# Optimization experiments

Measured on AMD Instinct MI355X. Metric: run time of the kernel, lower is better.

Reference implementation:

```python
import jax, jax.numpy as jnp
import numpy as np
from jax import lax

B, T, D, U, M = 64, 800, 3, 400, 20


def _lstm_peephole(x, Wx, Wh, b, p_i, p_f, p_o):
    """Peephole LSTM over [B,T,Din] -> [B,T,U]. Gate order: i,f,c,o."""
    xW = jnp.einsum('btd,dg->btg', x, Wx) + b  # precompute input projection [B,T,4U]
    h0 = jnp.zeros((x.shape[0], U), x.dtype)
    c0 = jnp.zeros((x.shape[0], U), x.dtype)

    def step(carry, xt):
        h, c = carry
        z = xt + h @ Wh
        zi, zf, zc, zo = jnp.split(z, 4, axis=-1)
        i = jax.nn.sigmoid(zi + p_i * c)
        f = jax.nn.sigmoid(zf + p_f * c)
        c_new = f * c + i * jnp.tanh(zc)
        o = jax.nn.sigmoid(zo + p_o * c_new)
        h_new = o * jnp.tanh(c_new)
        return (h_new, c_new), h_new

    _, hs = lax.scan(step, (h0, c0), jnp.swapaxes(xW, 0, 1))  # [T,B,U]
    return jnp.swapaxes(hs, 0, 1)


def _mdn(h, Wmdn, bmdn):
    y = h @ Wmdn + bmdn  # [B,T,6M+1]
    pi = jax.nn.softmax(y[..., :M], axis=-1)
    mu1 = y[..., M:2 * M]
    mu2 = y[..., 2 * M:3 * M]
    s1 = jnp.exp(y[..., 3 * M:4 * M])
    s2 = jnp.exp(y[..., 4 * M:5 * M])
    rho = jnp.tanh(y[..., 5 * M:6 * M])
    eos = jax.nn.sigmoid(y[..., 6 * M:])
    return jnp.concatenate([pi, mu1, mu2, s1, s2, rho, eos], axis=-1)


def setup_inputs() -> dict:
    key = jax.random.key(0)
    ks = jax.random.split(key, 32)
    s = 0.08
    inp = {'x': jax.random.normal(ks[0], (B, T, D), jnp.float32)}
    k = 1
    for l in range(3):
        din = D if l == 0 else D + U
        inp[f'Wx{l}'] = jax.random.normal(ks[k], (din, 4 * U), jnp.float32) * s; k += 1
        inp[f'Wh{l}'] = jax.random.normal(ks[k], (U, 4 * U), jnp.float32) * s; k += 1
        inp[f'b{l}'] = jnp.zeros((4 * U,), jnp.float32)
        inp[f'peep_i{l}'] = jax.random.normal(ks[k], (U,), jnp.float32) * s; k += 1
        inp[f'peep_f{l}'] = jax.random.normal(ks[k], (U,), jnp.float32) * s; k += 1
        inp[f'peep_o{l}'] = jax.random.normal(ks[k], (U,), jnp.float32) * s; k += 1
    inp['Wmdn'] = jax.random.normal(ks[k], (U, 6 * M + 1), jnp.float32) * s
    inp['bmdn'] = jnp.zeros((6 * M + 1,), jnp.float32)
    return inp


def reference(x, Wx0, Wh0, b0, peep_i0, peep_f0, peep_o0,
              Wx1, Wh1, b1, peep_i1, peep_f1, peep_o1,
              Wx2, Wh2, b2, peep_i2, peep_f2, peep_o2,
              Wmdn, bmdn):
    h = _lstm_peephole(x, Wx0, Wh0, b0, peep_i0, peep_f0, peep_o0)
    # skip connections: layers 1,2 take concat([inputs, prev_hidden])
    h = _lstm_peephole(jnp.concatenate([x, h], axis=-1), Wx1, Wh1, b1, peep_i1, peep_f1, peep_o1)
    h = _lstm_peephole(jnp.concatenate([x, h], axis=-1), Wx2, Wh2, b2, peep_i2, peep_f2, peep_o2)
    return _mdn(h, Wmdn, bmdn)
```

## Files before the change

kernel.cpp:

```cpp
#include <hip/hip_runtime.h>


#define TSTEPS 800
#define NG 4
#define GB 16
#define NSL 5
#define UB 80
#define CB 320
#define KP 416
#define RD 16
#define AS 424
#define ZS 332
#define ZIS 336

typedef __attribute__((ext_vector_type(8))) __bf16 bf16x8;
typedef __attribute__((ext_vector_type(4))) float floatx4;

struct Peeps { const float* pi[3]; const float* pf[3]; const float* po[3]; };

__device__ __forceinline__ unsigned short f2bf(float f) {
    unsigned int u = __float_as_uint(f);
    return (unsigned short)((u + 0x7FFFu + ((u >> 16) & 1u)) >> 16);
}
__device__ __forceinline__ float bf_lo(unsigned u) { return __uint_as_float(u << 16); }
__device__ __forceinline__ float bf_hi(unsigned u) { return __uint_as_float(u & 0xFFFF0000u); }
__device__ __forceinline__ float sigm_(float v) { return 1.f / (1.f + __expf(-v)); }
__device__ __forceinline__ float tanh_(float v) { float e = __expf(2.f * v); return 1.f - 2.f / (e + 1.f); }
__device__ __forceinline__ unsigned ld_a(const unsigned* p) {
    return __hip_atomic_load(p, __ATOMIC_RELAXED, __HIP_MEMORY_SCOPE_AGENT);
}
__device__ __forceinline__ void st_a(unsigned* p, unsigned v) {
    __hip_atomic_store(p, v, __ATOMIC_RELAXED, __HIP_MEMORY_SCOPE_AGENT);
}

__global__ void pack_rec(const float* __restrict__ Wx, const float* __restrict__ Wh,
                         const float* __restrict__ bias, unsigned short* __restrict__ dst,
                         int is_l0) {
    int idx = blockIdx.x * 256 + threadIdx.x;
    if (idx >= 1600 * KP) return;
    int col = idx / KP, k = idx - col * KP;
    int co = (col & 3) * 400 + (col >> 2);
    float v = 0.f;
    if (k < 400) v = Wh[k * 1600 + co];
    else if (is_l0) {
        if (k < 403) v = Wx[(k - 400) * 1600 + co];
        else if (k == 403) v = bias[co];
    }
    dst[idx] = f2bf(v);
}
__global__ void pack_pre(const float* __restrict__ Wx, const float* __restrict__ bias,
                         unsigned short* __restrict__ dst) {
    int idx = blockIdx.x * 256 + threadIdx.x;
    if (idx >= 1600 * KP) return;
    int col = idx / KP, k = idx - col * KP;
    int co = (col & 3) * 400 + (col >> 2);
    float v = 0.f;
    if (k < 400) v = Wx[(3 + k) * 1600 + co];
    else if (k < 403) v = Wx[(k - 400) * 1600 + co];
    else if (k == 403) v = bias[co];
    dst[idx] = f2bf(v);
}
__global__ void pack_x(const float* __restrict__ x, unsigned short* __restrict__ xp) {
    int idx = blockIdx.x * 256 + threadIdx.x;
    if (idx >= TSTEPS * 64) return;
    int t = idx / 64, b = idx - t * 64;
    unsigned short o[4];
    for (int d = 0; d < 3; ++d) o[d] = f2bf(x[(b * TSTEPS + t) * 3 + d]);
    o[3] = 0x3F80u;
    *(uint2*)(xp + (size_t)idx * 4) = *(uint2*)o;
}
__global__ void pack_mdn(const float* __restrict__ Wm, const float* __restrict__ bm,
                         unsigned short* __restrict__ dst) {
    int idx = blockIdx.x * 256 + threadIdx.x;
    if (idx >= 128 * KP) return;
    int col = idx / KP, k = idx - col * KP;
    float v = 0.f;
    if (col < 121) {
        if (k < 400) v = Wm[k * 121 + col];
        else if (k == 400) v = bm[col];
    }
    dst[idx] = f2bf(v);
}

__global__ __launch_bounds__(640)
void fused_scan(const unsigned short* __restrict__ Bp,
                const unsigned short* __restrict__ Bpre,
                const unsigned short* __restrict__ xpack,
                unsigned* __restrict__ ring,
                unsigned* __restrict__ zin,
                unsigned* __restrict__ seqb,
                unsigned short* __restrict__ h2,
                Peeps pp) {
    const int tid = threadIdx.x;
    const int lane = tid & 63;
    const int w = tid >> 6;
    const int bid = blockIdx.x;

    __shared__ unsigned short A[16 * AS];
    __shared__ float Z[16 * ZS];
    __shared__ unsigned short Zin[16 * ZIS];

    for (int i = tid; i < 16 * AS; i += 640) A[i] = 0;

    const int aoff = (lane & 15) * AS + ((lane >> 4) << 3);
    const int zc0 = w * 32 + (lane & 15);
    const int zr = (lane >> 4) << 2;
    const int er = tid / 40;
    const int up = tid - er * 40;

    if (bid < 60) {
        const int l = bid / 20;
        const int g = (bid % 20) / 5;
        const int s = bid % 5;
        bf16x8 breg[2][13];
        #pragma unroll
        for (int n = 0; n < 2; ++n) {
            const unsigned short* bpp = Bp + (size_t)l * 1600 * KP
                + (size_t)(s * CB + w * 32 + n * 16 + (lane & 15)) * KP + ((lane >> 4) << 3);
            #pragma unroll
            for (int kt = 0; kt < 13; ++kt) breg[n][kt] = *(const bf16x8*)(bpp + kt * 32);
        }
        unsigned* hs_own  = seqb + (l * NG + g) * 16;
        const unsigned* ps_up = seqb + 192 + ((l - 1) * NG + g) * 16;
        const unsigned* ps_dn = seqb + 192 + (l * NG + g) * 16;
        unsigned* ringL = ring + (size_t)(l * NG + g) * RD * 3200;
        const unsigned* zinL = zin + (size_t)((l - 1) * NG + g) * RD * 12800;

        const int ug0 = s * UB + 2 * up;
        const float pi0 = pp.pi[l][ug0], pi1 = pp.pi[l][ug0 + 1];
        const float pf0 = pp.pf[l][ug0], pf1 = pp.pf[l][ug0 + 1];
        const float po0 = pp.po[l][ug0], po1 = pp.po[l][ug0 + 1];
        float c0 = 0.f, c1 = 0.f;
        __syncthreads();

        for (int t = 0; t < TSTEPS; ++t) {
            if (w == 0) {
                const unsigned* fp = nullptr; unsigned need = 0;
                if (lane < 5)       { if (t > 0) { fp = hs_own + lane; need = (unsigned)t; } }
                else if (lane < 10) { if (l > 0) { fp = ps_up + (lane - 5); need = (unsigned)(t + 1); } }
                else if (lane < 15) { if (l < 2 && t >= 16 && (t & 7) == 0) { fp = ps_dn + (lane - 10); need = (unsigned)(t - 8); } }
                bool ok = (fp == nullptr) || (ld_a(fp) >= need);
                while (!__all(ok)) { if (!ok) ok = ld_a(fp) >= need; }
            }
            __syncthreads();

            if (t > 0) {
                const unsigned* src = ringL + (size_t)((t - 1) & 15) * 3200;
                for (int i = tid; i < 800; i += 640) {
                    int r = i / 50, c4 = (i - r * 50) * 4;
                    unsigned v0 = ld_a(src + r * 200 + c4);
                    unsigned v1 = ld_a(src + r * 200 + c4 + 1);
                    unsigned v2 = ld_a(src + r * 200 + c4 + 2);
                    unsigned v3 = ld_a(src + r * 200 + c4 + 3);
                    unsigned* dst = (unsigned*)&A[r * AS + c4 * 2];
                    dst[0] = v0; dst[1] = v1; dst[2] = v2; dst[3] = v3;
                }
            }
            if (l == 0 && tid < 16)
                *(uint2*)(&A[tid * AS + 400]) = *(const uint2*)(xpack + ((size_t)t * 64 + g * 16 + tid) * 4);
            if (l > 0) {
                const unsigned* zp = zinL + (size_t)(t & 15) * 12800 + er * 800 + s * 160 + up * 4;
                unsigned z0 = ld_a(zp), z1 = ld_a(zp + 1), z2 = ld_a(zp + 2), z3 = ld_a(zp + 3);
                unsigned* zd = (unsigned*)&Zin[er * ZIS + up * 8];
                zd[0] = z0; zd[1] = z1; zd[2] = z2; zd[3] = z3;
            }
            __syncthreads();

            floatx4 a0 = {0, 0, 0, 0}, a1 = {0, 0, 0, 0};
            #pragma unroll
            for (int kt = 0; kt < 13; ++kt) {
                bf16x8 a = *(const bf16x8*)(&A[aoff + kt * 32]);
                a0 = __builtin_amdgcn_mfma_f32_16x16x32_bf16(a, breg[0][kt], a0, 0, 0, 0);
                a1 = __builtin_amdgcn_mfma_f32_16x16x32_bf16(a, breg[1][kt], a1, 0, 0, 0);
            }
            #pragma unroll
            for (int ri = 0; ri < 4; ++ri) {
                Z[(zr + ri) * ZS + zc0] = a0[ri];
                Z[(zr + ri) * ZS + zc0 + 16] = a1[ri];
            }
            __syncthreads();

            {
                float4 za = *(const float4*)(&Z[er * ZS + 8 * up]);
                float4 zb = *(const float4*)(&Z[er * ZS + 8 * up + 4]);
                if (l > 0) {
                    const unsigned* q = (const unsigned*)&Zin[er * ZIS + 8 * up];
                    unsigned q0 = q[0], q1 = q[1], q2 = q[2], q3 = q[3];
                    za.x += bf_lo(q0); za.y += bf_hi(q0); za.z += bf_lo(q1); za.w += bf_hi(q1);
                    zb.x += bf_lo(q2); zb.y += bf_hi(q2); zb.z += bf_lo(q3); zb.w += bf_hi(q3);
                }
                float iv = sigm_(za.x + pi0 * c0);
                float fv = sigm_(za.y + pf0 * c0);
                float cn = fv * c0 + iv * tanh_(za.z);
                float ov = sigm_(za.w + po0 * cn);
                float h0 = ov * tanh_(cn);
                c0 = cn;
                iv = sigm_(zb.x + pi1 * c1);
                fv = sigm_(zb.y + pf1 * c1);
                cn = fv * c1 + iv * tanh_(zb.z);
                ov = sigm_(zb.w + po1 * cn);
                float h1 = ov * tanh_(cn);
                c1 = cn;
                unsigned packh = (unsigned)f2bf(h0) | ((unsigned)f2bf(h1) << 16);
                st_a(ringL + (size_t)(t & 15) * 3200 + er * 200 + s * 40 + up, packh);
                if (l == 2)
                    *(unsigned*)&h2[(size_t)t * 25600 + (g * GB + er) * 400 + ug0] = packh;
            }
            __syncthreads();
            if (tid == 0) st_a(hs_own + s, (unsigned)(t + 1));
        }
    } else {
        const int p = bid - 60;
        const int lp = 1 + p / 20;
        const int g = (p % 20) / 5;
        const int s = p % 5;
        bf16x8 breg[2][13];
        #pragma unroll
        for (int n = 0; n < 2; ++n) {
            const unsigned short* bpp = Bpre + (size_t)(lp - 1) * 1600 * KP
                + (size_t)(s * CB + w * 32 + n * 16 + (lane & 15)) * KP + ((lane >> 4) << 3);
            #pragma unroll
            for (int kt = 0; kt < 13; ++kt) breg[n][kt] = *(const bf16x8*)(bpp + kt * 32);
        }
        const unsigned* hs_up = seqb + ((lp - 1) * NG + g) * 16;
        const unsigned* hs_cons = seqb + (lp * NG + g) * 16;
        unsigned* pseq = seqb + 192 + ((lp - 1) * NG + g) * 16 + s;
        const unsigned* ringS = ring + (size_t)((lp - 1) * NG + g) * RD * 3200;
        unsigned* zinD = zin + (size_t)((lp - 1) * NG + g) * RD * 12800;
        __syncthreads();

        for (int t = 0; t < TSTEPS; ++t) {
            if (w == 0) {
                const unsigned* fp = nullptr; unsigned need = 0;
                if (lane < 5)       { fp = hs_up + lane; need = (unsigned)(t + 1); }
                else if (lane < 10) { if (t >= 16 && (t & 7) == 0) { fp = hs_cons + (lane - 5); need = (unsigned)(t - 8); } }
                bool ok = (fp == nullptr) || (ld_a(fp) >= need);
                while (!__all(ok)) { if (!ok) ok = ld_a(fp) >= need; }
            }
            __syncthreads();

            {
                const unsigned* src = ringS + (size_t)(t & 15) * 3200;
                for (int i = tid; i < 800; i += 640) {
                    int r = i / 50, c4 = (i - r * 50) * 4;
                    unsigned v0 = ld_a(src + r * 200 + c4);
                    unsigned v1 = ld_a(src + r * 200 + c4 + 1);
                    unsigned v2 = ld_a(src + r * 200 + c4 + 2);
                    unsigned v3 = ld_a(src + r * 200 + c4 + 3);
                    unsigned* dst = (unsigned*)&A[r * AS + c4 * 2];
                    dst[0] = v0; dst[1] = v1; dst[2] = v2; dst[3] = v3;
                }
            }
            if (tid < 16)
                *(uint2*)(&A[tid * AS + 400]) = *(const uint2*)(xpack + ((size_t)t * 64 + g * 16 + tid) * 4);
            __syncthreads();

            floatx4 a0 = {0, 0, 0, 0}, a1 = {0, 0, 0, 0};
            #pragma unroll
            for (int kt = 0; kt < 13; ++kt) {
                bf16x8 a = *(const bf16x8*)(&A[aoff + kt * 32]);
                a0 = __builtin_amdgcn_mfma_f32_16x16x32_bf16(a, breg[0][kt], a0, 0, 0, 0);
                a1 = __builtin_amdgcn_mfma_f32_16x16x32_bf16(a, breg[1][kt], a1, 0, 0, 0);
            }
            #pragma unroll
            for (int ri = 0; ri < 4; ++ri) {
                Z[(zr + ri) * ZS + zc0] = a0[ri];
                Z[(zr + ri) * ZS + zc0 + 16] = a1[ri];
            }
            __syncthreads();

            {
                float4 za = *(const float4*)(&Z[er * ZS + 8 * up]);
                float4 zb = *(const float4*)(&Z[er * ZS + 8 * up + 4]);
                unsigned* zd = zinD + (size_t)(t & 15) * 12800 + er * 800 + s * 160 + up * 4;
                st_a(zd,     (unsigned)f2bf(za.x) | ((unsigned)f2bf(za.y) << 16));
                st_a(zd + 1, (unsigned)f2bf(za.z) | ((unsigned)f2bf(za.w) << 16));
                st_a(zd + 2, (unsigned)f2bf(zb.x) | ((unsigned)f2bf(zb.y) << 16));
                st_a(zd + 3, (unsigned)f2bf(zb.z) | ((unsigned)f2bf(zb.w) << 16));
            }
            __syncthreads();
            if (tid == 0) st_a(pseq, (unsigned)(t + 1));
        }
    }
}

__global__ __launch_bounds__(256)
void mdn_kernel(const unsigned short* __restrict__ h2,
                const unsigned short* __restrict__ Bm,
                float* __restrict__ out) {
    const int blk = blockIdx.x;
    const int b = blk / 25;
    const int t0 = (blk - b * 25) * 32;
    const int tid = threadIdx.x;
    const int lane = tid & 63;
    const int w = tid >> 6;
    const int m = w & 1, nh = w >> 1;

    __shared__ unsigned short A[32 * 424];
    __shared__ float Z[32 * 132];
    __shared__ float rmax[32], rinv[32];

    for (int i = tid; i < 32 * 424; i += 256) A[i] = 0;
    __syncthreads();
    for (int c = tid; c < 32 * 50; c += 256) {
        int r = c / 50, j = c - r * 50;
        *(bf16x8*)(&A[r * 424 + j * 8]) = *(const bf16x8*)(h2 + (size_t)(t0 + r) * 25600 + b * 400 + j * 8);
    }
    if (tid < 32) A[tid * 424 + 400] = 0x3F80u;
    __syncthreads();

    floatx4 acc[4] = {{0,0,0,0},{0,0,0,0},{0,0,0,0},{0,0,0,0}};
    const int aoff = (m * 16 + (lane & 15)) * 424 + ((lane >> 4) << 3);
    #pragma unroll
    for (int kt = 0; kt < 13; ++kt) {
        bf16x8 a = *(const bf16x8*)(&A[aoff + kt * 32]);
        #pragma unroll
        for (int n = 0; n < 4; ++n) {
            const unsigned short* bp = Bm + (size_t)((nh * 4 + n) * 16 + (lane & 15)) * KP
                                          + ((lane >> 4) << 3) + kt * 32;
            acc[n] = __builtin_amdgcn_mfma_f32_16x16x32_bf16(a, *(const bf16x8*)bp, acc[n], 0, 0, 0);
        }
    }
    #pragma unroll
    for (int n = 0; n < 4; ++n) {
        int zc = (nh * 4 + n) * 16 + (lane & 15);
        int zrow = m * 16 + ((lane >> 4) << 2);
        #pragma unroll
        for (int ri = 0; ri < 4; ++ri)
            Z[(zrow + ri) * 132 + zc] = acc[n][ri];
    }
    __syncthreads();
    if (tid < 32) {
        float mx = -1e30f;
        for (int j = 0; j < 20; ++j) mx = fmaxf(mx, Z[tid * 132 + j]);
        float sm = 0.f;
        for (int j = 0; j < 20; ++j) sm += __expf(Z[tid * 132 + j] - mx);
        rmax[tid] = mx;
        rinv[tid] = 1.f / sm;
    }
    __syncthreads();
    for (int idx = tid; idx < 32 * 121; idx += 256) {
        int r = idx / 121, jo = idx - r * 121;
        float v = Z[r * 132 + jo];
        float o;
        if (jo < 20) o = __expf(v - rmax[r]) * rinv[r];
        else if (jo < 60) o = v;
        else if (jo < 100) o = __expf(v);
        else if (jo < 120) o = tanh_(v);
        else o = sigm_(v);
        out[(size_t)(b * TSTEPS + t0 + r) * 121 + jo] = o;
    }
}

extern "C" void kernel_launch(void* const* d_in, const int* in_sizes, int n_in,
                              void* d_out, int out_size, void* d_ws, size_t ws_size,
                              hipStream_t stream) {
    const float* x = (const float*)d_in[0];
    const float* Wx[3] = {(const float*)d_in[1], (const float*)d_in[7], (const float*)d_in[13]};
    const float* Wh[3] = {(const float*)d_in[2], (const float*)d_in[8], (const float*)d_in[14]};
    const float* bb[3] = {(const float*)d_in[3], (const float*)d_in[9], (const float*)d_in[15]};
    Peeps pp;
    for (int l = 0; l < 3; ++l) {
        pp.pi[l] = (const float*)d_in[4 + 6 * l];
        pp.pf[l] = (const float*)d_in[5 + 6 * l];
        pp.po[l] = (const float*)d_in[6 + 6 * l];
    }
    const float* Wm = (const float*)d_in[19];
    const float* bm = (const float*)d_in[20];
    float* out = (float*)d_out;

    char* base = (char*)d_ws;
    size_t off = 0;
    auto alloc = [&](size_t bytes) -> void* {
        void* r = base + off;
        off = (off + bytes + 255) & ~(size_t)255;
        return r;
    };
    unsigned* seqb        = (unsigned*)alloc(320 * sizeof(unsigned));
    unsigned* ring        = (unsigned*)alloc((size_t)3 * NG * RD * 3200 * 4);
    unsigned* zin         = (unsigned*)alloc((size_t)2 * NG * RD * 12800 * 4);
    unsigned short* Bp    = (unsigned short*)alloc((size_t)3 * 1600 * KP * 2);
    unsigned short* Bpre  = (unsigned short*)alloc((size_t)2 * 1600 * KP * 2);
    unsigned short* Bm    = (unsigned short*)alloc((size_t)128 * KP * 2);
    unsigned short* xpk   = (unsigned short*)alloc((size_t)TSTEPS * 64 * 4 * 2);
    unsigned short* h2    = (unsigned short*)alloc((size_t)TSTEPS * 64 * 400 * 2);

    hipMemsetAsync(seqb, 0, 320 * sizeof(unsigned), stream);

    for (int l = 0; l < 3; ++l)
        pack_rec<<<2600, 256, 0, stream>>>(Wx[l], Wh[l], bb[l], Bp + (size_t)l * 1600 * KP, l == 0);
    pack_pre<<<2600, 256, 0, stream>>>(Wx[1], bb[1], Bpre);
    pack_pre<<<2600, 256, 0, stream>>>(Wx[2], bb[2], Bpre + (size_t)1600 * KP);
    pack_x<<<200, 256, 0, stream>>>(x, xpk);
    pack_mdn<<<208, 256, 0, stream>>>(Wm, bm, Bm);

    fused_scan<<<100, 640, 0, stream>>>(Bp, Bpre, xpk, ring, zin, seqb, h2, pp);

    mdn_kernel<<<1600, 256, 0, stream>>>(h2, Bm, out);
}
```

Measured before the change: 3.771 ms.

## Replace per-step sequence flags with tagged hidden-state exchange and batch pre-projection by two

Recurrent blocks now publish each hidden value together with a timestep tag in a small 4-deep exchange buffer. Consumers poll the tagged data directly, which removes the separate flag round-trip and one barrier per step. Each block also writes its own slice of h into LDS locally, and the next x input is prefetched one step ahead. The pre-projection blocks now handle two timesteps per iteration with coarser flags, and the zin load goes straight to registers instead of staging through LDS. The cost is more polling traffic, a larger memset, and more complex ordering that relies on relaxed atomics for correctness.

```diff
diff --git a/kernel.cpp b/kernel.cpp
--- a/kernel.cpp
+++ b/kernel.cpp
@@ -9,9 +9,9 @@
 #define CB 320
 #define KP 416
 #define RD 16
+#define HXD 4
 #define AS 424
 #define ZS 332
-#define ZIS 336
 
 typedef __attribute__((ext_vector_type(8))) __bf16 bf16x8;
 typedef __attribute__((ext_vector_type(4))) float floatx4;
@@ -86,27 +86,27 @@
 void fused_scan(const unsigned short* __restrict__ Bp,
                 const unsigned short* __restrict__ Bpre,
                 const unsigned short* __restrict__ xpack,
-                unsigned* __restrict__ ring,
+                unsigned* __restrict__ hx,
+                unsigned* __restrict__ hring,
                 unsigned* __restrict__ zin,
                 unsigned* __restrict__ seqb,
-                unsigned short* __restrict__ h2,
+                unsigned* __restrict__ h2,
                 Peeps pp) {
     const int tid = threadIdx.x;
     const int lane = tid & 63;
     const int w = tid >> 6;
     const int bid = blockIdx.x;
 
-    __shared__ unsigned short A[16 * AS];
+    __shared__ unsigned short A[32 * AS];
     __shared__ float Z[16 * ZS];
-    __shared__ unsigned short Zin[16 * ZIS];
-
-    for (int i = tid; i < 16 * AS; i += 640) A[i] = 0;
-
+
+    for (int i = tid; i < 32 * AS; i += 640) A[i] = 0;
+
+    const int er = tid / 40;
+    const int up = tid - er * 40;
     const int aoff = (lane & 15) * AS + ((lane >> 4) << 3);
     const int zc0 = w * 32 + (lane & 15);
     const int zr = (lane >> 4) << 2;
-    const int er = tid / 40;
-    const int up = tid - er * 40;
 
     if (bid < 60) {
         const int l = bid / 20;
@@ -120,51 +120,67 @@
             #pragma unroll
             for (int kt = 0; kt < 13; ++kt) breg[n][kt] = *(const bf16x8*)(bpp + kt * 32);
         }
-        unsigned* hs_own  = seqb + (l * NG + g) * 16;
-        const unsigned* ps_up = seqb + 192 + ((l - 1) * NG + g) * 16;
-        const unsigned* ps_dn = seqb + 192 + (l * NG + g) * 16;
-        unsigned* ringL = ring + (size_t)(l * NG + g) * RD * 3200;
+        unsigned* hxL = hx + (size_t)(l * NG + g) * HXD * 6400;
+        unsigned* ringL = hring + (size_t)(l * NG + g) * RD * 3200;
         const unsigned* zinL = zin + (size_t)((l - 1) * NG + g) * RD * 12800;
-
+        unsigned* FHown = seqb + ((l * NG + g) * NSL + s) * 16;
+        const unsigned* FZup = seqb + (60 + ((l - 1) * NG + g) * NSL) * 16;
+        const unsigned* FZdn = seqb + (60 + (l * NG + g) * NSL) * 16;
+
+        const int p0 = ((s + 1) % 5) * 80, p1 = ((s + 2) % 5) * 80;
+        const int p2 = ((s + 3) % 5) * 80, p3 = ((s + 4) % 5) * 80;
         const int ug0 = s * UB + 2 * up;
         const float pi0 = pp.pi[l][ug0], pi1 = pp.pi[l][ug0 + 1];
         const float pf0 = pp.pf[l][ug0], pf1 = pp.pf[l][ug0 + 1];
         const float po0 = pp.po[l][ug0], po1 = pp.po[l][ug0 + 1];
         float c0 = 0.f, c1 = 0.f;
+
         __syncthreads();
+        if (l == 0 && tid < 16)
+            *(uint2*)(&A[tid * AS + 400]) = *(const uint2*)(xpack + ((size_t)0 * 64 + g * 16 + tid) * 4);
+        __syncthreads();
 
         for (int t = 0; t < TSTEPS; ++t) {
-            if (w == 0) {
-                const unsigned* fp = nullptr; unsigned need = 0;
-                if (lane < 5)       { if (t > 0) { fp = hs_own + lane; need = (unsigned)t; } }
-                else if (lane < 10) { if (l > 0) { fp = ps_up + (lane - 5); need = (unsigned)(t + 1); } }
-                else if (lane < 15) { if (l < 2 && t >= 16 && (t & 7) == 0) { fp = ps_dn + (lane - 10); need = (unsigned)(t - 8); } }
-                bool ok = (fp == nullptr) || (ld_a(fp) >= need);
-                while (!__all(ok)) { if (!ok) ok = ld_a(fp) >= need; }
+            {
+                const unsigned want = (unsigned)(t - 1) << 16;
+                const unsigned* hb = hxL + (size_t)((t + 3) & 3) * 6400 + er * 400 + 2 * up;
+                const unsigned* fp = nullptr; unsigned fneed = 0;
+                if (l > 0 && (t & 3) == 0 && tid < NSL) { fp = FZup + tid * 16; fneed = (unsigned)(t + 4); }
+                else if (l < 2 && (t & 7) == 0 && tid >= NSL && tid < 2 * NSL) {
+                    fp = FZdn + (tid - NSL) * 16; fneed = (unsigned)(t > 8 ? t - 8 : 0);
+                }
+                unsigned v0, v1, v2, v3, v4, v5, v6, v7;
+                for (;;) {
+                    bool ok = true;
+                    if (t > 0) {
+                        v0 = ld_a(hb + p0); v1 = ld_a(hb + p0 + 1);
+                        v2 = ld_a(hb + p1); v3 = ld_a(hb + p1 + 1);
+                        v4 = ld_a(hb + p2); v5 = ld_a(hb + p2 + 1);
+                        v6 = ld_a(hb + p3); v7 = ld_a(hb + p3 + 1);
+                        ok = ((v0 & 0xFFFF0000u) == want) & ((v1 & 0xFFFF0000u) == want) &
+                             ((v2 & 0xFFFF0000u) == want) & ((v3 & 0xFFFF0000u) == want) &
+                             ((v4 & 0xFFFF0000u) == want) & ((v5 & 0xFFFF0000u) == want) &
+                             ((v6 & 0xFFFF0000u) == want) & ((v7 & 0xFFFF0000u) == want);
+                    }
+                    if (fp) ok &= (ld_a(fp) >= fneed);
+                    if (__all(ok)) break;
+                }
+                if (t > 0) {
+                    const int ab = er * AS + 2 * up;
+                    *(unsigned*)&A[ab + p0] = (v0 & 0xFFFFu) | (v1 << 16);
+                    *(unsigned*)&A[ab + p1] = (v2 & 0xFFFFu) | (v3 << 16);
+                    *(unsigned*)&A[ab + p2] = (v4 & 0xFFFFu) | (v5 << 16);
+                    *(unsigned*)&A[ab + p3] = (v6 & 0xFFFFu) | (v7 << 16);
+                }
             }
             __syncthreads();
-
-            if (t > 0) {
-                const unsigned* src = ringL + (size_t)((t - 1) & 15) * 3200;
-                for (int i = tid; i < 800; i += 640) {
-                    int r = i / 50, c4 = (i - r * 50) * 4;
-                    unsigned v0 = ld_a(src + r * 200 + c4);
-                    unsigned v1 = ld_a(src + r * 200 + c4 + 1);
-                    unsigned v2 = ld_a(src + r * 200 + c4 + 2);
-                    unsigned v3 = ld_a(src + r * 200 + c4 + 3);
-                    unsigned* dst = (unsigned*)&A[r * AS + c4 * 2];
-                    dst[0] = v0; dst[1] = v1; dst[2] = v2; dst[3] = v3;
-                }
-            }
-            if (l == 0 && tid < 16)
-                *(uint2*)(&A[tid * AS + 400]) = *(const uint2*)(xpack + ((size_t)t * 64 + g * 16 + tid) * 4);
+            if (tid == 0) st_a(FHown, (unsigned)t);
+
+            unsigned q0, q1, q2, q3;
             if (l > 0) {
-                const unsigned* zp = zinL + (size_t)(t & 15) * 12800 + er * 800 + s * 160 + up * 4;
-                unsigned z0 = ld_a(zp), z1 = ld_a(zp + 1), z2 = ld_a(zp + 2), z3 = ld_a(zp + 3);
-                unsigned* zd = (unsigned*)&Zin[er * ZIS + up * 8];
-                zd[0] = z0; zd[1] = z1; zd[2] = z2; zd[3] = z3;
-            }
-            __syncthreads();
+                const unsigned* zp = zinL + (size_t)(t & 15) * 12800 + er * 800 + 4 * (s * 40 + up);
+                q0 = ld_a(zp); q1 = ld_a(zp + 1); q2 = ld_a(zp + 2); q3 = ld_a(zp + 3);
+            }
 
             floatx4 a0 = {0, 0, 0, 0}, a1 = {0, 0, 0, 0};
             #pragma unroll
@@ -180,107 +196,114 @@
             }
             __syncthreads();
 
-            {
-                float4 za = *(const float4*)(&Z[er * ZS + 8 * up]);
-                float4 zb = *(const float4*)(&Z[er * ZS + 8 * up + 4]);
-                if (l > 0) {
-                    const unsigned* q = (const unsigned*)&Zin[er * ZIS + 8 * up];
-                    unsigned q0 = q[0], q1 = q[1], q2 = q[2], q3 = q[3];
-                    za.x += bf_lo(q0); za.y += bf_hi(q0); za.z += bf_lo(q1); za.w += bf_hi(q1);
-                    zb.x += bf_lo(q2); zb.y += bf_hi(q2); zb.z += bf_lo(q3); zb.w += bf_hi(q3);
-                }
-                float iv = sigm_(za.x + pi0 * c0);
-                float fv = sigm_(za.y + pf0 * c0);
-                float cn = fv * c0 + iv * tanh_(za.z);
-                float ov = sigm_(za.w + po0 * cn);
-                float h0 = ov * tanh_(cn);
-                c0 = cn;
-                iv = sigm_(zb.x + pi1 * c1);
-                fv = sigm_(zb.y + pf1 * c1);
-                cn = fv * c1 + iv * tanh_(zb.z);
-                ov = sigm_(zb.w + po1 * cn);
-                float h1 = ov * tanh_(cn);
-                c1 = cn;
-                unsigned packh = (unsigned)f2bf(h0) | ((unsigned)f2bf(h1) << 16);
+            float4 za = *(const float4*)(&Z[er * ZS + 8 * up]);
+            float4 zb4 = *(const float4*)(&Z[er * ZS + 8 * up + 4]);
+            if (l > 0) {
+                za.x += bf_lo(q0); za.y += bf_hi(q0); za.z += bf_lo(q1); za.w += bf_hi(q1);
+                zb4.x += bf_lo(q2); zb4.y += bf_hi(q2); zb4.z += bf_lo(q3); zb4.w += bf_hi(q3);
+            }
+            float iv = sigm_(za.x + pi0 * c0);
+            float fv = sigm_(za.y + pf0 * c0);
+            float cn = fv * c0 + iv * tanh_(za.z);
+            float ov = sigm_(za.w + po0 * cn);
+            float h0 = ov * tanh_(cn);
+            c0 = cn;
+            iv = sigm_(zb4.x + pi1 * c1);
+            fv = sigm_(zb4.y + pf1 * c1);
+            cn = fv * c1 + iv * tanh_(zb4.z);
+            ov = sigm_(zb4.w + po1 * cn);
+            float h1 = ov * tanh_(cn);
+            c1 = cn;
+            unsigned packh = (unsigned)f2bf(h0) | ((unsigned)f2bf(h1) << 16);
+            *(unsigned*)&A[er * AS + ug0] = packh;
+            if (l == 0 && tid < 16 && t + 1 < TSTEPS)
+                *(uint2*)(&A[tid * AS + 400]) = *(const uint2*)(xpack + ((size_t)(t + 1) * 64 + g * 16 + tid) * 4);
+            __syncthreads();
+
+            unsigned* hxs = hxL + (size_t)(t & 3) * 6400 + er * 400 + ug0;
+            st_a(hxs, ((unsigned)t << 16) | (packh & 0xFFFFu));
+            st_a(hxs + 1, ((unsigned)t << 16) | (packh >> 16));
+            if (l < 2)
                 st_a(ringL + (size_t)(t & 15) * 3200 + er * 200 + s * 40 + up, packh);
-                if (l == 2)
-                    *(unsigned*)&h2[(size_t)t * 25600 + (g * GB + er) * 400 + ug0] = packh;
-            }
-            __syncthreads();
-            if (tid == 0) st_a(hs_own + s, (unsigned)(t + 1));
+            else
+                h2[(size_t)t * 12800 + (g * GB + er) * 200 + s * 40 + up] = packh;
         }
+        __syncthreads();
+        if (tid == 0) st_a(FHown, (unsigned)TSTEPS);
     } else {
         const int p = bid - 60;
-        const int lp = 1 + p / 20;
+        const int lz = p / 20;
         const int g = (p % 20) / 5;
-        const int s = p % 5;
+        const int sp = p % 5;
         bf16x8 breg[2][13];
         #pragma unroll
         for (int n = 0; n < 2; ++n) {
-            const unsigned short* bpp = Bpre + (size_t)(lp - 1) * 1600 * KP
-                + (size_t)(s * CB + w * 32 + n * 16 + (lane & 15)) * KP + ((lane >> 4) << 3);
+            const unsigned short* bpp = Bpre + (size_t)lz * 1600 * KP
+                + (size_t)(sp * CB + w * 32 + n * 16 + (lane & 15)) * KP + ((lane >> 4) << 3);
             #pragma unroll
             for (int kt = 0; kt < 13; ++kt) breg[n][kt] = *(const bf16x8*)(bpp + kt * 32);
         }
-        const unsigned* hs_up = seqb + ((lp - 1) * NG + g) * 16;
-        const unsigned* hs_cons = seqb + (lp * NG + g) * 16;
-        unsigned* pseq = seqb + 192 + ((lp - 1) * NG + g) * 16 + s;
-        const unsigned* ringS = ring + (size_t)((lp - 1) * NG + g) * RD * 3200;
-        unsigned* zinD = zin + (size_t)((lp - 1) * NG + g) * RD * 12800;
+        const unsigned* ringS = hring + (size_t)(lz * NG + g) * RD * 3200;
+        unsigned* zinD = zin + (size_t)(lz * NG + g) * RD * 12800;
+        const unsigned* FHup = seqb + ((lz * NG + g) * NSL) * 16;
+        const unsigned* FHdn = seqb + (((lz + 1) * NG + g) * NSL) * 16;
+        unsigned* FZown = seqb + (60 + (lz * NG + g) * NSL + sp) * 16;
         __syncthreads();
 
-        for (int t = 0; t < TSTEPS; ++t) {
-            if (w == 0) {
+        for (int c = 0; c < TSTEPS; c += 2) {
+            {
                 const unsigned* fp = nullptr; unsigned need = 0;
-                if (lane < 5)       { fp = hs_up + lane; need = (unsigned)(t + 1); }
-                else if (lane < 10) { if (t >= 16 && (t & 7) == 0) { fp = hs_cons + (lane - 5); need = (unsigned)(t - 8); } }
+                if (tid < NSL) { fp = FHup + tid * 16; need = (unsigned)(c + 2); }
+                else if (tid < 2 * NSL) { fp = FHdn + (tid - NSL) * 16; need = (unsigned)(c > 14 ? c - 14 : 0); }
                 bool ok = (fp == nullptr) || (ld_a(fp) >= need);
                 while (!__all(ok)) { if (!ok) ok = ld_a(fp) >= need; }
             }
             __syncthreads();
-
-            {
-                const unsigned* src = ringS + (size_t)(t & 15) * 3200;
-                for (int i = tid; i < 800; i += 640) {
-                    int r = i / 50, c4 = (i - r * 50) * 4;
-                    unsigned v0 = ld_a(src + r * 200 + c4);
-                    unsigned v1 = ld_a(src + r * 200 + c4 + 1);
-                    unsigned v2 = ld_a(src + r * 200 + c4 + 2);
-                    unsigned v3 = ld_a(src + r * 200 + c4 + 3);
-                    unsigned* dst = (unsigned*)&A[r * AS + c4 * 2];
-                    dst[0] = v0; dst[1] = v1; dst[2] = v2; dst[3] = v3;
+            if (tid == 0 && c > 0) st_a(FZown, (unsigned)c);
+
+            for (int i = tid; i < 6400; i += 640) {
+                int tc = i / 3200, j = i - tc * 3200;
+                unsigned v = ld_a(ringS + (size_t)((c + tc) & 15) * 3200 + j);
+                int r = j / 200, d = j - r * 200;
+                *(unsigned*)&A[(tc * 16 + r) * AS + 2 * d] = v;
+            }
+            if (tid < 32) {
+                int tc = tid >> 4, r = tid & 15;
+                *(uint2*)(&A[(tc * 16 + r) * AS + 400]) =
+                    *(const uint2*)(xpack + ((size_t)(c + tc) * 64 + g * 16 + r) * 4);
+            }
+            __syncthreads();
+
+            floatx4 a00 = {0,0,0,0}, a01 = {0,0,0,0}, a10 = {0,0,0,0}, a11 = {0,0,0,0};
+            #pragma unroll
+            for (int kt = 0; kt < 13; ++kt) {
+                bf16x8 x0 = *(const bf16x8*)(&A[aoff + kt * 32]);
+                bf16x8 x1 = *(const bf16x8*)(&A[aoff + 16 * AS + kt * 32]);
+                a00 = __builtin_amdgcn_mfma_f32_16x16x32_bf16(x0, breg[0][kt], a00, 0, 0, 0);
+                a01 = __builtin_amdgcn_mfma_f32_16x16x32_bf16(x0, breg[1][kt], a01, 0, 0, 0);
+                a10 = __builtin_amdgcn_mfma_f32_16x16x32_bf16(x1, breg[0][kt], a10, 0, 0, 0);
+                a11 = __builtin_amdgcn_mfma_f32_16x16x32_bf16(x1, breg[1][kt], a11, 0, 0, 0);
+            }
+            #pragma unroll
+            for (int m = 0; m < 2; ++m) {
+                #pragma unroll
+                for (int ri = 0; ri < 4; ++ri) {
+                    Z[(zr + ri) * ZS + zc0] = (m ? a10[ri] : a00[ri]);
+                    Z[(zr + ri) * ZS + zc0 + 16] = (m ? a11[ri] : a01[ri]);
                 }
-            }
-            if (tid < 16)
-                *(uint2*)(&A[tid * AS + 400]) = *(const uint2*)(xpack + ((size_t)t * 64 + g * 16 + tid) * 4);
-            __syncthreads();
-
-            floatx4 a0 = {0, 0, 0, 0}, a1 = {0, 0, 0, 0};
-            #pragma unroll
-            for (int kt = 0; kt < 13; ++kt) {
-                bf16x8 a = *(const bf16x8*)(&A[aoff + kt * 32]);
-                a0 = __builtin_amdgcn_mfma_f32_16x16x32_bf16(a, breg[0][kt], a0, 0, 0, 0);
-                a1 = __builtin_amdgcn_mfma_f32_16x16x32_bf16(a, breg[1][kt], a1, 0, 0, 0);
-            }
-            #pragma unroll
-            for (int ri = 0; ri < 4; ++ri) {
-                Z[(zr + ri) * ZS + zc0] = a0[ri];
-                Z[(zr + ri) * ZS + zc0 + 16] = a1[ri];
-            }
-            __syncthreads();
-
-            {
+                __syncthreads();
                 float4 za = *(const float4*)(&Z[er * ZS + 8 * up]);
-                float4 zb = *(const float4*)(&Z[er * ZS + 8 * up + 4]);
-                unsigned* zd = zinD + (size_t)(t & 15) * 12800 + er * 800 + s * 160 + up * 4;
-                st_a(zd,     (unsigned)f2bf(za.x) | ((unsigned)f2bf(za.y) << 16));
-                st_a(zd + 1, (unsigned)f2bf(za.z) | ((unsigned)f2bf(za.w) << 16));
-                st_a(zd + 2, (unsigned)f2bf(zb.x) | ((unsigned)f2bf(zb.y) << 16));
-                st_a(zd + 3, (unsigned)f2bf(zb.z) | ((unsigned)f2bf(zb.w) << 16));
-            }
-            __syncthreads();
-            if (tid == 0) st_a(pseq, (unsigned)(t + 1));
+                float4 zbv = *(const float4*)(&Z[er * ZS + 8 * up + 4]);
+                unsigned* zg = zinD + (size_t)((c + m) & 15) * 12800 + er * 800 + sp * 160 + 4 * up;
+                st_a(zg,     (unsigned)f2bf(za.x) | ((unsigned)f2bf(za.y) << 16));
+                st_a(zg + 1, (unsigned)f2bf(za.z) | ((unsigned)f2bf(za.w) << 16));
+                st_a(zg + 2, (unsigned)f2bf(zbv.x) | ((unsigned)f2bf(zbv.y) << 16));
+                st_a(zg + 3, (unsigned)f2bf(zbv.z) | ((unsigned)f2bf(zbv.w) << 16));
+                __syncthreads();
+            }
         }
+        __syncthreads();
+        if (tid == 0) st_a(FZown, (unsigned)TSTEPS);
     }
 }
 
@@ -376,8 +399,9 @@
         off = (off + bytes + 255) & ~(size_t)255;
         return r;
     };
-    unsigned* seqb        = (unsigned*)alloc(320 * sizeof(unsigned));
-    unsigned* ring        = (unsigned*)alloc((size_t)3 * NG * RD * 3200 * 4);
+    unsigned* seqb        = (unsigned*)alloc(1600 * sizeof(unsigned));
+    unsigned* hx          = (unsigned*)alloc((size_t)3 * NG * HXD * 6400 * 4);
+    unsigned* hring       = (unsigned*)alloc((size_t)3 * NG * RD * 3200 * 4);
     unsigned* zin         = (unsigned*)alloc((size_t)2 * NG * RD * 12800 * 4);
     unsigned short* Bp    = (unsigned short*)alloc((size_t)3 * 1600 * KP * 2);
     unsigned short* Bpre  = (unsigned short*)alloc((size_t)2 * 1600 * KP * 2);
@@ -385,7 +409,8 @@
     unsigned short* xpk   = (unsigned short*)alloc((size_t)TSTEPS * 64 * 4 * 2);
     unsigned short* h2    = (unsigned short*)alloc((size_t)TSTEPS * 64 * 400 * 2);
 
-    hipMemsetAsync(seqb, 0, 320 * sizeof(unsigned), stream);
+    hipMemsetAsync(seqb, 0, 1600 * sizeof(unsigned), stream);
+    hipMemsetAsync(hx, 0xAA, (size_t)3 * NG * HXD * 6400 * 4, stream);
 
     for (int l = 0; l < 3; ++l)
         pack_rec<<<2600, 256, 0, stream>>>(Wx[l], Wh[l], bb[l], Bp + (size_t)l * 1600 * KP, l == 0);
@@ -394,7 +419,8 @@
     pack_x<<<200, 256, 0, stream>>>(x, xpk);
     pack_mdn<<<208, 256, 0, stream>>>(Wm, bm, Bm);
 
-    fused_scan<<<100, 640, 0, stream>>>(Bp, Bpre, xpk, ring, zin, seqb, h2, pp);
+    fused_scan<<<100, 640, 0, stream>>>(Bp, Bpre, xpk, hx, hring, zin, seqb,
+                                        (unsigned*)h2, pp);
 
     mdn_kernel<<<1600, 256, 0, stream>>>(h2, Bm, out);
 }
```

New measurement: 3.034 ms. 1.24x faster.
